# Performance work log

Measured on AMD Instinct MI355X. Metric: run time of the kernel, lower is better.

The kernel has to match this reference:

```python
import jax, jax.numpy as jnp
import numpy as np

SENS = 200
DM = 128
NMAPS = 2
NLAYERS = 2
TH = 0.01
EPS = 1e-5
BATCH = 8
SEQ = 96
HEADS = 8


def setup_inputs() -> dict:
    key = jax.random.key(0)
    ks = jax.random.split(key, 8)
    x = jax.random.normal(ks[0], (BATCH, SENS, SEQ, DM), jnp.float32)
    attn_s = jax.random.uniform(ks[1], (1, BATCH, HEADS, SENS, SENS), jnp.float32)
    supports = jax.random.uniform(ks[2], (SENS, SENS), jnp.float32)
    W_conv = jax.random.normal(ks[3], (NMAPS, NLAYERS, DM, DM), jnp.float32) * 0.05
    b_conv = jnp.zeros((NMAPS, NLAYERS, DM), jnp.float32)
    bn_gamma = jnp.ones((NMAPS, DM), jnp.float32)
    bn_beta = jnp.zeros((NMAPS, DM), jnp.float32)
    W_out = jax.random.normal(ks[4], (NMAPS * DM, DM), jnp.float32) * 0.05
    b_out = jnp.zeros((DM,), jnp.float32)
    return dict(x=x, attn_s=attn_s, supports=supports, W_conv=W_conv,
                b_conv=b_conv, bn_gamma=bn_gamma, bn_beta=bn_beta,
                W_out=W_out, b_out=b_out)


def _process_map(A):
    # make_symmetric: lower triangle + mirrored strict lower triangle
    A = jnp.tril(A) + jnp.tril(A, -1).T
    # clamp: threshold on absolute value; note original returns |A| thresholded
    Aa = jnp.abs(A)
    A = jnp.where(Aa > TH, Aa, jnp.zeros_like(Aa))
    # SparseTensor.from_dense(A).t()
    return A.T


def _gcn_norm(adj_t):
    # GCNConv default: add self-loops (weight 1), symmetric D^-1/2 A D^-1/2
    A = adj_t + jnp.eye(adj_t.shape[0], dtype=adj_t.dtype)
    deg = A.sum(axis=1)
    d = jnp.where(deg > 0, jax.lax.rsqrt(deg), jnp.zeros_like(deg))
    return d[:, None] * A * d[None, :]


def reference(x, attn_s, supports, W_conv, b_conv, bn_gamma, bn_beta, W_out, b_out):
    B, N, S, D = x.shape
    # reshape_mat: [B,N,S,D] -> [B*S, N, D]
    xr = x.transpose(0, 2, 1, 3).reshape(B * S, N, D)

    # supports: [data map, adaptive map from attention (mean over batch, heads)]
    maps = [_process_map(supports), _process_map(attn_s[0].mean(axis=(0, 1)))]

    gcn_outputs = []
    for i in range(NMAPS):
        An = _gcn_norm(maps[i])  # [N,N]
        h = jnp.zeros_like(xr[..., :1]) * 0.0  # placeholder replaced below
        h = None
        for l in range(NLAYERS):
            xw = jnp.einsum('bnf,fg->bng', xr, W_conv[i, l])
            hl = jnp.einsum('mn,bng->bmg', An, xw) + b_conv[i, l]
            h = hl if h is None else h + hl
        # BatchNorm1d over feature channel (training-mode batch stats, biased var)
        mu = h.mean(axis=(0, 1))
        var = h.var(axis=(0, 1))
        hn = (h - mu) * jax.lax.rsqrt(var + EPS) * bn_gamma[i] + bn_beta[i]
        gcn_outputs.append(jax.nn.relu(hn))

    cat = jnp.concatenate(gcn_outputs, axis=-1)  # [B*S, N, NMAPS*DM]
    y = jax.nn.relu(jnp.einsum('bnc,cd->bnd', cat, W_out) + b_out)
    # inverse_reshape_mat: [B*S, N, D] -> [B, N, S, D]
    return y.reshape(B, S, N, D).transpose(0, 2, 1, 3)
```

## Files before the change

kernel.cpp:

```cpp
#include <hip/hip_runtime.h>

#define SENS 200
#define DM 128
#define SEQ 96
#define NB 8
#define BS 768
#define NTOT 153600
#define TH 0.01f
#define BN_EPS 1e-5f
#define MPAD 224
#define XWROW 236
#define ASROW 76

typedef __attribute__((ext_vector_type(8)))  __bf16 bf16x8;
typedef __attribute__((ext_vector_type(4)))  __bf16 bf16x4;
typedef __attribute__((ext_vector_type(16))) float  f32x16;

__device__ __forceinline__ f32x16 mfma32(bf16x8 a, bf16x8 b, f32x16 c) {
    return __builtin_amdgcn_mfma_f32_32x32x16_bf16(a, b, c, 0, 0, 0);
}
__device__ __forceinline__ bf16x8 join8(bf16x4 a, bf16x4 b) {
    bf16x8 r;
    #pragma unroll
    for (int j = 0; j < 4; ++j) { r[j] = a[j]; r[j + 4] = b[j]; }
    return r;
}

__global__ void attn_mean_kernel(const float* __restrict__ attn, float* __restrict__ mapA) {
    int idx = blockIdx.x * 256 + threadIdx.x;
    if (idx >= SENS * SENS) return;
    float s = 0.f;
    #pragma unroll 8
    for (int q = 0; q < 64; ++q) s += attn[(size_t)q * SENS * SENS + idx];
    mapA[idx] = s * (1.0f / 64.0f);
}

__global__ void build_map_kernel(const float* __restrict__ supports, const float* __restrict__ mapA,
                                 float* __restrict__ M, float* __restrict__ deg) {
    __shared__ float red[256];
    int m = blockIdx.x, map = blockIdx.y, j = threadIdx.x;
    const float* src = (map == 0) ? supports : mapA;
    float v = 0.f;
    if (j < SENS) {
        float sym = (m >= j) ? src[m * SENS + j] : src[j * SENS + m];
        float a = fabsf(sym);
        v = (a > TH) ? a : 0.f;
        M[(size_t)map * SENS * SENS + m * SENS + j] = v;
    }
    red[j] = v;
    __syncthreads();
    for (int off = 128; off > 0; off >>= 1) {
        if (j < off) red[j] += red[j + off];
        __syncthreads();
    }
    if (j == 0) deg[map * SENS + m] = red[0] + 1.0f;
}

__global__ void anbf_kernel(const float* __restrict__ M, const float* __restrict__ deg,
                            __bf16* __restrict__ Anb) {
    const int m = blockIdx.x, map = blockIdx.y, j = threadIdx.x;
    if (j >= MPAD) return;
    float val = 0.f;
    if (m < SENS && j < SENS) {
        float a = M[((size_t)map * SENS + m) * SENS + j] + ((m == j) ? 1.f : 0.f);
        val = rsqrtf(deg[map * SENS + m]) * a * rsqrtf(deg[map * SENS + j]);
    }
    Anb[(((size_t)map * 14 + (j >> 4)) * MPAD + m) * 16 + (j & 15)] = (__bf16)val;
}

__global__ void prepw_kernel(const float* __restrict__ W_conv, const float* __restrict__ b_conv,
                             const float* __restrict__ W_out,
                             __bf16* __restrict__ Wt, __bf16* __restrict__ Wot,
                             float* __restrict__ bsum, float* __restrict__ bnacc) {
    const int idx = blockIdx.x * 256 + threadIdx.x;
    if (idx < 32768) {
        const int map = idx >> 14, g = (idx >> 7) & 127, f = idx & 127;
        const float* wp = W_conv + (size_t)map * 2 * DM * DM + f * DM + g;
        Wt[(((size_t)map * 8 + (f >> 4)) * DM + g) * 16 + (f & 15)] = (__bf16)(wp[0] + wp[DM * DM]);
    } else if (idx < 65536) {
        const int k = idx - 32768, d = k >> 8, c = k & 255;
        Wot[(((size_t)(c >> 4)) * DM + d) * 16 + (c & 15)] = (__bf16)W_out[c * DM + d];
    } else if (idx < 65792) {
        const int k = idx - 65536, map = k >> 7, g = k & 127;
        bsum[k] = b_conv[(map * 2) * DM + g] + b_conv[(map * 2 + 1) * DM + g];
    } else if (idx < 66304) {
        bnacc[idx - 65792] = 0.f;
    }
}

__global__ void xk_kernel(const float* __restrict__ x, __bf16* __restrict__ xk) {
    const int bs = blockIdx.x;
    const int b = bs / SEQ, s = bs % SEQ;
    const int t = threadIdx.x, f = t & 127, nh = t >> 7;
    __bf16* xo = xk + ((size_t)bs * 8 + (f >> 4)) * MPAD * 16 + (f & 15);
    const float* xp = x + ((size_t)b * SENS) * SEQ * DM + (size_t)s * DM + f;
    for (int n0 = 0; n0 < MPAD; n0 += 2) {
        const int n = n0 + nh;
        float v = (n < SENS) ? xp[(size_t)n * SEQ * DM] : 0.f;
        xo[(size_t)n * 16] = (__bf16)v;
    }
}

__global__ __launch_bounds__(448) void conv_kernel(
    const __bf16* __restrict__ xk, const __bf16* __restrict__ Anb,
    const __bf16* __restrict__ Wt, const float* __restrict__ bsum,
    __bf16* __restrict__ h, float* __restrict__ bnacc)
{
    __shared__ __bf16 xw[128 * XWROW];
    const int bs = blockIdx.x, map = blockIdx.y;
    const int t = threadIdx.x, w = t >> 6, lane = t & 63;
    const int l31 = lane & 31, hi = lane >> 5;

    {
        f32x16 acc[4];
        #pragma unroll
        for (int gs = 0; gs < 4; ++gs)
            #pragma unroll
            for (int r = 0; r < 16; ++r) acc[gs][r] = 0.f;
        const __bf16* xb = xk + (((size_t)bs * 8) * MPAD + w * 32 + l31) * 16 + hi * 8;
        const __bf16* wb = Wt + (((size_t)map * 8) * DM + l31) * 16 + hi * 8;
        #pragma unroll
        for (int kc = 0; kc < 8; ++kc) {
            bf16x8 bfrag = *(const bf16x8*)(xb + (size_t)kc * MPAD * 16);
            #pragma unroll
            for (int gs = 0; gs < 4; ++gs) {
                bf16x8 afrag = *(const bf16x8*)(wb + ((size_t)kc * DM + gs * 32) * 16);
                acc[gs] = mfma32(afrag, bfrag, acc[gs]);
            }
        }
        #pragma unroll
        for (int gs = 0; gs < 4; ++gs)
            #pragma unroll
            for (int r = 0; r < 16; ++r) {
                const int row = gs * 32 + (r & 3) + 8 * (r >> 2) + 4 * hi;
                xw[row * XWROW + w * 32 + l31] = (__bf16)acc[gs][r];
            }
    }
    __syncthreads();

    f32x16 acc2[4];
    #pragma unroll
    for (int ct = 0; ct < 4; ++ct)
        #pragma unroll
        for (int r = 0; r < 16; ++r) acc2[ct][r] = 0.f;
    {
        const __bf16* ab = Anb + (((size_t)map * 14) * MPAD + w * 32 + l31) * 16 + hi * 8;
        for (int kc = 0; kc < 14; ++kc) {
            bf16x8 afrag = *(const bf16x8*)(ab + (size_t)kc * MPAD * 16);
            #pragma unroll
            for (int ct = 0; ct < 4; ++ct) {
                const __bf16* p = &xw[(ct * 32 + l31) * XWROW + kc * 16 + hi * 8];
                bf16x8 bfrag = join8(*(const bf16x4*)p, *(const bf16x4*)(p + 4));
                acc2[ct] = mfma32(afrag, bfrag, acc2[ct]);
            }
        }
    }
    float bsn[4], bsq[4];
    #pragma unroll
    for (int ct = 0; ct < 4; ++ct) {
        const float bias = bsum[map * DM + ct * 32 + l31];
        bf16x8 h0, h1;
        float s = 0.f, q = 0.f;
        #pragma unroll
        for (int r = 0; r < 16; ++r) {
            const float v = acc2[ct][r] + bias;
            if (r < 8) h0[r] = (__bf16)v; else h1[r - 8] = (__bf16)v;
            const int m = w * 32 + (r & 3) + 8 * (r >> 2) + 4 * hi;
            if (m < SENS) { s += v; q += v * v; }
        }
        __bf16* hp = h + ((((size_t)(bs * 2 + map) * 7 + w) * 4 + ct) * 64 + lane) * 16;
        *(bf16x8*)hp = h0;
        *(bf16x8*)(hp + 8) = h1;
        s += __shfl_xor(s, 32);
        q += __shfl_xor(q, 32);
        bsn[ct] = s; bsq[ct] = q;
    }
    __syncthreads();
    float* red = (float*)xw;
    if (hi == 0) {
        #pragma unroll
        for (int ct = 0; ct < 4; ++ct) {
            red[(ct * 32 + l31) * 7 + w] = bsn[ct];
            red[(128 + ct * 32 + l31) * 7 + w] = bsq[ct];
        }
    }
    __syncthreads();
    if (t < 256) {
        const int sq = t >> 7, g = t & 127;
        float s = 0.f;
        #pragma unroll
        for (int k = 0; k < 7; ++k) s += red[(sq * 128 + g) * 7 + k];
        atomicAdd(&bnacc[sq * 256 + map * DM + g], s);
    }
}

__global__ void bnfin_kernel(const float* __restrict__ bnacc,
                             const float* __restrict__ gamma, const float* __restrict__ beta,
                             float* __restrict__ scale, float* __restrict__ shift) {
    int t = threadIdx.x;
    float mu = bnacc[t] * (1.f / (float)NTOT);
    float var = bnacc[256 + t] * (1.f / (float)NTOT) - mu * mu;
    float sc = gamma[t] * rsqrtf(var + BN_EPS);
    scale[t] = sc;
    shift[t] = beta[t] - mu * sc;
}

__global__ __launch_bounds__(512) void out_kernel(
    const __bf16* __restrict__ h, const __bf16* __restrict__ Wot,
    const float* __restrict__ scale, const float* __restrict__ shift,
    const float* __restrict__ b_out, float* __restrict__ out)
{
    __shared__ __bf16 As[MPAD * ASROW];
    __shared__ float sc_s[256], sh_s[256];
    const int bs = blockIdx.x;
    const int b = bs / SEQ, s = bs % SEQ;
    const int t = threadIdx.x, w = t >> 6, lane = t & 63;
    const int l31 = lane & 31, hi = lane >> 5;
    const int dct = w & 3, sbase = w >> 2;
    if (t < 256) { sc_s[t] = scale[t]; sh_s[t] = shift[t]; }

    f32x16 acc[4];
    {
        const float bo = b_out[dct * 32 + l31];
        #pragma unroll
        for (int i = 0; i < 4; ++i)
            #pragma unroll
            for (int r = 0; r < 16; ++r) acc[i][r] = bo;
    }
    for (int chunk = 0; chunk < 4; ++chunk) {
        const int map = chunk >> 1;
        __syncthreads();
        {
            const __bf16* hb = h + ((size_t)(bs * 2 + map) * 28 + (chunk & 1) * 2) * 1024;
            #pragma unroll
            for (int it = 0; it < 4; ++it) {
                const int idx = it * 512 + t;
                if (idx < 1792) {
                    const int half = idx & 1, lane_s = (idx >> 1) & 63;
                    const int ctl = (idx >> 7) & 1, strip = idx >> 8;
                    bf16x8 v = *(const bf16x8*)(hb + ((size_t)strip * 4 + ctl) * 1024 + lane_s * 16 + half * 8);
                    const int cl = ctl * 32 + (lane_s & 31);
                    const int cg = map * DM + (chunk & 1) * 64 + cl;
                    const float scv = sc_s[cg], shv = sh_s[cg];
                    const int mbase = strip * 32 + 4 * (lane_s >> 5) + 16 * half;
                    #pragma unroll
                    for (int q2 = 0; q2 < 8; ++q2) {
                        const int row = mbase + (q2 & 3) + 8 * (q2 >> 2);
                        const float fv = (float)v[q2] * scv + shv;
                        As[row * ASROW + cl] = (__bf16)fmaxf(fv, 0.f);
                    }
                }
            }
        }
        __syncthreads();
        #pragma unroll
        for (int kc = 0; kc < 4; ++kc) {
            bf16x8 bfrag = *(const bf16x8*)(Wot + (((size_t)(chunk * 4 + kc)) * DM + dct * 32 + l31) * 16 + hi * 8);
            #pragma unroll
            for (int i = 0; i < 4; ++i) {
                const int strip = sbase + 2 * i;
                if (strip >= 7) break;
                const __bf16* ap = &As[(strip * 32 + l31) * ASROW + kc * 16 + hi * 8];
                bf16x8 afrag = join8(*(const bf16x4*)ap, *(const bf16x4*)(ap + 4));
                acc[i] = mfma32(afrag, bfrag, acc[i]);
            }
        }
    }
    #pragma unroll
    for (int i = 0; i < 4; ++i) {
        const int strip = sbase + 2 * i;
        if (strip >= 7) break;
        #pragma unroll
        for (int r = 0; r < 16; ++r) {
            const int m = strip * 32 + (r & 3) + 8 * (r >> 2) + 4 * hi;
            if (m < SENS)
                out[(((size_t)b * SENS + m) * SEQ + s) * DM + dct * 32 + l31] = fmaxf(acc[i][r], 0.f);
        }
    }
}

extern "C" void kernel_launch(void* const* d_in, const int* in_sizes, int n_in,
                              void* d_out, int out_size, void* d_ws, size_t ws_size,
                              hipStream_t stream) {
    const float* x        = (const float*)d_in[0];
    const float* attn     = (const float*)d_in[1];
    const float* supports = (const float*)d_in[2];
    const float* W_conv   = (const float*)d_in[3];
    const float* b_conv   = (const float*)d_in[4];
    const float* gamma    = (const float*)d_in[5];
    const float* beta     = (const float*)d_in[6];
    const float* W_out    = (const float*)d_in[7];
    const float* b_out    = (const float*)d_in[8];
    float* out = (float*)d_out;
    char* base = (char*)d_ws;

    float*  mapA  = (float*)(base + 0);
    float*  Mbuf  = (float*)(base + 160000);
    float*  deg   = (float*)(base + 480000);
    float*  bnacc = (float*)(base + 481664);
    float*  scale = (float*)(base + 483712);
    float*  shiftv= (float*)(base + 484736);
    float*  bsum  = (float*)(base + 485760);
    __bf16* Wt    = (__bf16*)(base + 486784);
    __bf16* Wot   = (__bf16*)(base + 552320);
    __bf16* Anb   = (__bf16*)(base + 617856);
    __bf16* xk    = (__bf16*)(base + 1048576);
    __bf16* h     = (__bf16*)(base + 45088768);

    attn_mean_kernel<<<157, 256, 0, stream>>>(attn, mapA);
    build_map_kernel<<<dim3(SENS, 2), 256, 0, stream>>>(supports, mapA, Mbuf, deg);
    anbf_kernel<<<dim3(MPAD, 2), 256, 0, stream>>>(Mbuf, deg, Anb);
    prepw_kernel<<<260, 256, 0, stream>>>(W_conv, b_conv, W_out, Wt, Wot, bsum, bnacc);
    xk_kernel<<<BS, 256, 0, stream>>>(x, xk);
    conv_kernel<<<dim3(BS, 2), 448, 0, stream>>>(xk, Anb, Wt, bsum, h, bnacc);
    bnfin_kernel<<<1, 256, 0, stream>>>(bnacc, gamma, beta, scale, shiftv);
    out_kernel<<<BS, 512, 0, stream>>>(h, Wot, scale, shiftv, b_out, out);
}
```

Before: 312.1 us.

## Merge prep kernels, vectorize x repack, trim K padding, fold BN finalize

Merges the adjacency-normalization, weight-prep and x-repack kernels into one launch. The x repack now uses float4 loads and bf16x4 stores. The conv kernel cuts the adjacency K dimension from 224 to 208 (13 chunks), shrinks the LDS row stride, and splits the MFMA accumulators into halves to lower register pressure. The BN finalize kernel is removed and its scale/shift math is recomputed per block in out_kernel. This saves two launches and some padded MFMA work, at the cost of redundant per-block BN math and a more complex fused prep kernel.

New measurement: 282.9 us. -9.4%, faster.

```diff
diff --git a/kernel.cpp b/kernel.cpp
--- a/kernel.cpp
+++ b/kernel.cpp
@@ -9,7 +9,8 @@
 #define TH 0.01f
 #define BN_EPS 1e-5f
 #define MPAD 224
-#define XWROW 236
+#define KP 208
+#define XWROW 212
 #define ASROW 76
 
 typedef __attribute__((ext_vector_type(8)))  __bf16 bf16x8;
@@ -56,48 +57,53 @@
     if (j == 0) deg[map * SENS + m] = red[0] + 1.0f;
 }
 
-__global__ void anbf_kernel(const float* __restrict__ M, const float* __restrict__ deg,
-                            __bf16* __restrict__ Anb) {
-    const int m = blockIdx.x, map = blockIdx.y, j = threadIdx.x;
-    if (j >= MPAD) return;
-    float val = 0.f;
-    if (m < SENS && j < SENS) {
-        float a = M[((size_t)map * SENS + m) * SENS + j] + ((m == j) ? 1.f : 0.f);
-        val = rsqrtf(deg[map * SENS + m]) * a * rsqrtf(deg[map * SENS + j]);
-    }
-    Anb[(((size_t)map * 14 + (j >> 4)) * MPAD + m) * 16 + (j & 15)] = (__bf16)val;
-}
-
-__global__ void prepw_kernel(const float* __restrict__ W_conv, const float* __restrict__ b_conv,
-                             const float* __restrict__ W_out,
-                             __bf16* __restrict__ Wt, __bf16* __restrict__ Wot,
-                             float* __restrict__ bsum, float* __restrict__ bnacc) {
-    const int idx = blockIdx.x * 256 + threadIdx.x;
-    if (idx < 32768) {
-        const int map = idx >> 14, g = (idx >> 7) & 127, f = idx & 127;
-        const float* wp = W_conv + (size_t)map * 2 * DM * DM + f * DM + g;
-        Wt[(((size_t)map * 8 + (f >> 4)) * DM + g) * 16 + (f & 15)] = (__bf16)(wp[0] + wp[DM * DM]);
-    } else if (idx < 65536) {
-        const int k = idx - 32768, d = k >> 8, c = k & 255;
-        Wot[(((size_t)(c >> 4)) * DM + d) * 16 + (c & 15)] = (__bf16)W_out[c * DM + d];
-    } else if (idx < 65792) {
-        const int k = idx - 65536, map = k >> 7, g = k & 127;
-        bsum[k] = b_conv[(map * 2) * DM + g] + b_conv[(map * 2 + 1) * DM + g];
-    } else if (idx < 66304) {
-        bnacc[idx - 65792] = 0.f;
-    }
-}
-
-__global__ void xk_kernel(const float* __restrict__ x, __bf16* __restrict__ xk) {
-    const int bs = blockIdx.x;
-    const int b = bs / SEQ, s = bs % SEQ;
-    const int t = threadIdx.x, f = t & 127, nh = t >> 7;
-    __bf16* xo = xk + ((size_t)bs * 8 + (f >> 4)) * MPAD * 16 + (f & 15);
-    const float* xp = x + ((size_t)b * SENS) * SEQ * DM + (size_t)s * DM + f;
-    for (int n0 = 0; n0 < MPAD; n0 += 2) {
-        const int n = n0 + nh;
-        float v = (n < SENS) ? xp[(size_t)n * SEQ * DM] : 0.f;
-        xo[(size_t)n * 16] = (__bf16)v;
+__global__ __launch_bounds__(256) void prep2_kernel(
+    const float* __restrict__ x, const float* __restrict__ M, const float* __restrict__ deg,
+    const float* __restrict__ W_conv, const float* __restrict__ b_conv,
+    const float* __restrict__ W_out,
+    __bf16* __restrict__ xk, __bf16* __restrict__ Anb,
+    __bf16* __restrict__ Wt, __bf16* __restrict__ Wot,
+    float* __restrict__ bsum, float* __restrict__ bnacc)
+{
+    const int bid = blockIdx.x, t = threadIdx.x;
+    if (bid < BS) {
+        const int bs = bid, b = bs / SEQ, s = bs % SEQ;
+        const int fq = t & 31, sub = t >> 5;
+        const float* xp = x + ((size_t)b * SENS) * SEQ * DM + (size_t)s * DM + fq * 4;
+        __bf16* xo = xk + ((size_t)bs * 8 + (fq >> 2)) * MPAD * 16 + (fq & 3) * 4;
+        for (int n = sub; n < MPAD; n += 8) {
+            float4 v = make_float4(0.f, 0.f, 0.f, 0.f);
+            if (n < SENS) v = *(const float4*)(xp + (size_t)n * SEQ * DM);
+            bf16x4 o;
+            o[0] = (__bf16)v.x; o[1] = (__bf16)v.y; o[2] = (__bf16)v.z; o[3] = (__bf16)v.w;
+            *(bf16x4*)(xo + (size_t)n * 16) = o;
+        }
+    } else if (bid < BS + 2 * MPAD) {
+        const int i = bid - BS, map = i / MPAD, m = i % MPAD;
+        const int j = t;
+        if (j < KP) {
+            float val = 0.f;
+            if (m < SENS && j < SENS) {
+                float a = M[((size_t)map * SENS + m) * SENS + j] + ((m == j) ? 1.f : 0.f);
+                val = rsqrtf(deg[map * SENS + m]) * a * rsqrtf(deg[map * SENS + j]);
+            }
+            Anb[(((size_t)map * 13 + (j >> 4)) * MPAD + m) * 16 + (j & 15)] = (__bf16)val;
+        }
+    } else {
+        const int idx = (bid - (BS + 2 * MPAD)) * 256 + t;
+        if (idx < 32768) {
+            const int map = idx >> 14, g = (idx >> 7) & 127, f = idx & 127;
+            const float* wp = W_conv + (size_t)map * 2 * DM * DM + f * DM + g;
+            Wt[(((size_t)map * 8 + (f >> 4)) * DM + g) * 16 + (f & 15)] = (__bf16)(wp[0] + wp[DM * DM]);
+        } else if (idx < 65536) {
+            const int k = idx - 32768, d = k >> 8, c = k & 255;
+            Wot[(((size_t)(c >> 4)) * DM + d) * 16 + (c & 15)] = (__bf16)W_out[c * DM + d];
+        } else if (idx < 65792) {
+            const int k = idx - 65536, map = k >> 7, g = k & 127;
+            bsum[k] = b_conv[(map * 2) * DM + g] + b_conv[(map * 2 + 1) * DM + g];
+        } else if (idx < 66304) {
+            bnacc[idx - 65792] = 0.f;
+        }
     }
 }
 
@@ -111,69 +117,72 @@
     const int t = threadIdx.x, w = t >> 6, lane = t & 63;
     const int l31 = lane & 31, hi = lane >> 5;
 
-    {
-        f32x16 acc[4];
-        #pragma unroll
-        for (int gs = 0; gs < 4; ++gs)
-            #pragma unroll
-            for (int r = 0; r < 16; ++r) acc[gs][r] = 0.f;
-        const __bf16* xb = xk + (((size_t)bs * 8) * MPAD + w * 32 + l31) * 16 + hi * 8;
-        const __bf16* wb = Wt + (((size_t)map * 8) * DM + l31) * 16 + hi * 8;
+    const __bf16* xb = xk + (((size_t)bs * 8) * MPAD + w * 32 + l31) * 16 + hi * 8;
+    #pragma unroll
+    for (int gh = 0; gh < 2; ++gh) {
+        f32x16 acc[2];
+        #pragma unroll
+        for (int p = 0; p < 2; ++p)
+            #pragma unroll
+            for (int r = 0; r < 16; ++r) acc[p][r] = 0.f;
+        const __bf16* wb = Wt + (((size_t)map * 8) * DM + gh * 64 + l31) * 16 + hi * 8;
         #pragma unroll
         for (int kc = 0; kc < 8; ++kc) {
             bf16x8 bfrag = *(const bf16x8*)(xb + (size_t)kc * MPAD * 16);
             #pragma unroll
-            for (int gs = 0; gs < 4; ++gs) {
-                bf16x8 afrag = *(const bf16x8*)(wb + ((size_t)kc * DM + gs * 32) * 16);
-                acc[gs] = mfma32(afrag, bfrag, acc[gs]);
-            }
-        }
-        #pragma unroll
-        for (int gs = 0; gs < 4; ++gs)
+            for (int p = 0; p < 2; ++p)
+                acc[p] = mfma32(*(const bf16x8*)(wb + ((size_t)kc * DM + p * 32) * 16), bfrag, acc[p]);
+        }
+        if (w < 6 || l31 < 16) {
+            #pragma unroll
+            for (int p = 0; p < 2; ++p)
+                #pragma unroll
+                for (int r = 0; r < 16; ++r) {
+                    const int row = gh * 64 + p * 32 + (r & 3) + 8 * (r >> 2) + 4 * hi;
+                    xw[row * XWROW + w * 32 + l31] = (__bf16)acc[p][r];
+                }
+        }
+    }
+    __syncthreads();
+
+    float bsn[4], bsq[4];
+    const __bf16* ab = Anb + (((size_t)map * 13) * MPAD + w * 32 + l31) * 16 + hi * 8;
+    #pragma unroll
+    for (int cth = 0; cth < 2; ++cth) {
+        f32x16 acc2[2];
+        #pragma unroll
+        for (int p = 0; p < 2; ++p)
+            #pragma unroll
+            for (int r = 0; r < 16; ++r) acc2[p][r] = 0.f;
+        #pragma unroll
+        for (int kc = 0; kc < 13; ++kc) {
+            bf16x8 afrag = *(const bf16x8*)(ab + (size_t)kc * MPAD * 16);
+            #pragma unroll
+            for (int p = 0; p < 2; ++p) {
+                const __bf16* pp = &xw[((cth * 2 + p) * 32 + l31) * XWROW + kc * 16 + hi * 8];
+                acc2[p] = mfma32(afrag, join8(*(const bf16x4*)pp, *(const bf16x4*)(pp + 4)), acc2[p]);
+            }
+        }
+        #pragma unroll
+        for (int p = 0; p < 2; ++p) {
+            const int ct = cth * 2 + p;
+            const float bias = bsum[map * DM + ct * 32 + l31];
+            bf16x8 h0, h1;
+            float s = 0.f, q = 0.f;
             #pragma unroll
             for (int r = 0; r < 16; ++r) {
-                const int row = gs * 32 + (r & 3) + 8 * (r >> 2) + 4 * hi;
-                xw[row * XWROW + w * 32 + l31] = (__bf16)acc[gs][r];
-            }
-    }
-    __syncthreads();
-
-    f32x16 acc2[4];
-    #pragma unroll
-    for (int ct = 0; ct < 4; ++ct)
-        #pragma unroll
-        for (int r = 0; r < 16; ++r) acc2[ct][r] = 0.f;
-    {
-        const __bf16* ab = Anb + (((size_t)map * 14) * MPAD + w * 32 + l31) * 16 + hi * 8;
-        for (int kc = 0; kc < 14; ++kc) {
-            bf16x8 afrag = *(const bf16x8*)(ab + (size_t)kc * MPAD * 16);
-            #pragma unroll
-            for (int ct = 0; ct < 4; ++ct) {
-                const __bf16* p = &xw[(ct * 32 + l31) * XWROW + kc * 16 + hi * 8];
-                bf16x8 bfrag = join8(*(const bf16x4*)p, *(const bf16x4*)(p + 4));
-                acc2[ct] = mfma32(afrag, bfrag, acc2[ct]);
-            }
-        }
-    }
-    float bsn[4], bsq[4];
-    #pragma unroll
-    for (int ct = 0; ct < 4; ++ct) {
-        const float bias = bsum[map * DM + ct * 32 + l31];
-        bf16x8 h0, h1;
-        float s = 0.f, q = 0.f;
-        #pragma unroll
-        for (int r = 0; r < 16; ++r) {
-            const float v = acc2[ct][r] + bias;
-            if (r < 8) h0[r] = (__bf16)v; else h1[r - 8] = (__bf16)v;
-            const int m = w * 32 + (r & 3) + 8 * (r >> 2) + 4 * hi;
-            if (m < SENS) { s += v; q += v * v; }
-        }
-        __bf16* hp = h + ((((size_t)(bs * 2 + map) * 7 + w) * 4 + ct) * 64 + lane) * 16;
-        *(bf16x8*)hp = h0;
-        *(bf16x8*)(hp + 8) = h1;
-        s += __shfl_xor(s, 32);
-        q += __shfl_xor(q, 32);
-        bsn[ct] = s; bsq[ct] = q;
+                const float v = acc2[p][r] + bias;
+                if (r < 8) h0[r] = (__bf16)v; else h1[r - 8] = (__bf16)v;
+                const int m = w * 32 + (r & 3) + 8 * (r >> 2) + 4 * hi;
+                if (m < SENS) { s += v; q += v * v; }
+            }
+            __bf16* hp = h + ((((size_t)(bs * 2 + map) * 7 + w) * 4 + ct) * 64 + lane) * 16;
+            *(bf16x8*)hp = h0;
+            *(bf16x8*)(hp + 8) = h1;
+            s += __shfl_xor(s, 32);
+            q += __shfl_xor(q, 32);
+            bsn[ct] = s; bsq[ct] = q;
+        }
     }
     __syncthreads();
     float* red = (float*)xw;
@@ -194,20 +203,10 @@
     }
 }
 
-__global__ void bnfin_kernel(const float* __restrict__ bnacc,
-                             const float* __restrict__ gamma, const float* __restrict__ beta,
-                             float* __restrict__ scale, float* __restrict__ shift) {
-    int t = threadIdx.x;
-    float mu = bnacc[t] * (1.f / (float)NTOT);
-    float var = bnacc[256 + t] * (1.f / (float)NTOT) - mu * mu;
-    float sc = gamma[t] * rsqrtf(var + BN_EPS);
-    scale[t] = sc;
-    shift[t] = beta[t] - mu * sc;
-}
-
 __global__ __launch_bounds__(512) void out_kernel(
     const __bf16* __restrict__ h, const __bf16* __restrict__ Wot,
-    const float* __restrict__ scale, const float* __restrict__ shift,
+    const float* __restrict__ bnacc,
+    const float* __restrict__ gamma, const float* __restrict__ beta,
     const float* __restrict__ b_out, float* __restrict__ out)
 {
     __shared__ __bf16 As[MPAD * ASROW];
@@ -217,7 +216,13 @@
     const int t = threadIdx.x, w = t >> 6, lane = t & 63;
     const int l31 = lane & 31, hi = lane >> 5;
     const int dct = w & 3, sbase = w >> 2;
-    if (t < 256) { sc_s[t] = scale[t]; sh_s[t] = shift[t]; }
+    if (t < 256) {
+        const float mu = bnacc[t] * (1.f / (float)NTOT);
+        const float var = bnacc[256 + t] * (1.f / (float)NTOT) - mu * mu;
+        const float sc = gamma[t] * rsqrtf(var + BN_EPS);
+        sc_s[t] = sc;
+        sh_s[t] = beta[t] - mu * sc;
+    }
 
     f32x16 acc[4];
     {
@@ -261,8 +266,7 @@
                 const int strip = sbase + 2 * i;
                 if (strip >= 7) break;
                 const __bf16* ap = &As[(strip * 32 + l31) * ASROW + kc * 16 + hi * 8];
-                bf16x8 afrag = join8(*(const bf16x4*)ap, *(const bf16x4*)(ap + 4));
-                acc[i] = mfma32(afrag, bfrag, acc[i]);
+                acc[i] = mfma32(join8(*(const bf16x4*)ap, *(const bf16x4*)(ap + 4)), bfrag, acc[i]);
             }
         }
     }
@@ -298,21 +302,17 @@
     float*  Mbuf  = (float*)(base + 160000);
     float*  deg   = (float*)(base + 480000);
     float*  bnacc = (float*)(base + 481664);
-    float*  scale = (float*)(base + 483712);
-    float*  shiftv= (float*)(base + 484736);
-    float*  bsum  = (float*)(base + 485760);
-    __bf16* Wt    = (__bf16*)(base + 486784);
-    __bf16* Wot   = (__bf16*)(base + 552320);
-    __bf16* Anb   = (__bf16*)(base + 617856);
+    float*  bsum  = (float*)(base + 483712);
+    __bf16* Wt    = (__bf16*)(base + 484736);
+    __bf16* Wot   = (__bf16*)(base + 550272);
+    __bf16* Anb   = (__bf16*)(base + 615808);
     __bf16* xk    = (__bf16*)(base + 1048576);
     __bf16* h     = (__bf16*)(base + 45088768);
 
     attn_mean_kernel<<<157, 256, 0, stream>>>(attn, mapA);
     build_map_kernel<<<dim3(SENS, 2), 256, 0, stream>>>(supports, mapA, Mbuf, deg);
-    anbf_kernel<<<dim3(MPAD, 2), 256, 0, stream>>>(Mbuf, deg, Anb);
-    prepw_kernel<<<260, 256, 0, stream>>>(W_conv, b_conv, W_out, Wt, Wot, bsum, bnacc);
-    xk_kernel<<<BS, 256, 0, stream>>>(x, xk);
+    prep2_kernel<<<BS + 2 * MPAD + 260, 256, 0, stream>>>(x, Mbuf, deg, W_conv, b_conv, W_out,
+                                                          xk, Anb, Wt, Wot, bsum, bnacc);
     conv_kernel<<<dim3(BS, 2), 448, 0, stream>>>(xk, Anb, Wt, bsum, h, bnacc);
-    bnfin_kernel<<<1, 256, 0, stream>>>(bnacc, gamma, beta, scale, shiftv);
-    out_kernel<<<BS, 512, 0, stream>>>(h, Wot, scale, shiftv, b_out, out);
-}
+    out_kernel<<<BS, 512, 0, stream>>>(h, Wot, bnacc, gamma, beta, b_out, out);
+}
```
